# Performance work log

Measured on AMD Instinct MI355X. Metric: run time of the kernel, lower is better.

## Reference

```python
import jax, jax.numpy as jnp
import numpy as np

# Module constants (from init_kwargs)
K_BUDGET = 16      # selector budget K
R_REFRAC = 1       # refractory separation r
LAM = 0.5          # selector regularization lambda
MAX_PROXY = 64     # max_proxy_points (K_eff cap)


def setup_inputs() -> dict:
    key = jax.random.key(0)
    ks = jax.random.split(key, 8)
    B, T, D = 32, 4096, 128
    H, K_LIFT, D_MODEL = 256, 64, 1024
    g = lambda i, shape, s=0.05: jax.random.normal(ks[i], shape, jnp.float32) * s
    return {
        "x": jax.random.normal(ks[0], (B, T, D), jnp.float32),
        "W1": g(1, (D, H)),
        "b1": jnp.zeros((H,), jnp.float32),
        "w_e": g(2, (H,)),
        "w_s": g(3, (H,)),
        "W_lift": g(4, (D + 3, K_LIFT)),
        "b_lift": jnp.zeros((K_LIFT,), jnp.float32),
        "W_proj": g(5, (K_LIFT, D_MODEL)),
        "b_proj": jnp.zeros((D_MODEL,), jnp.float32),
        "log_temperature": jnp.zeros((), jnp.float32),
    }


def _soft_selector(saliency, log_temperature):
    """SoftSelectorProxy.forward: sigmoid relaxation of budget+refractory QP."""
    T = saliency.shape[1]
    temp = jnp.clip(jnp.exp(log_temperature), 0.1, 10.0)
    logits = (saliency / (2.0 * LAM) - 0.5) / temp
    y = jax.nn.sigmoid(logits)
    y = y.at[:, 0].set(0.0)
    budget = jnp.clip(y.sum(axis=1, keepdims=True), 1e-6)
    y = y * jnp.minimum(K_BUDGET / budget, 1.0)
    for d in range(1, min(R_REFRAC + 1, T)):  # r=1 -> single unrolled step
        pair_sum = y + jnp.roll(y, -d, axis=1)
        y = y * jnp.minimum(2.0 / (1.0 + pair_sum), 1.0)
    y = y.at[:, 0].set(0.0)
    return y


def reference(x, W1, b1, w_e, w_s, W_lift, b_lift, W_proj, b_proj, log_temperature):
    B, T, D = x.shape
    # 1. CausalEventModel: per-step MLP -> event scores + saliency  [B,T]
    h = jnp.tanh(jnp.einsum("btd,dh->bth", x, W1) + b1)
    event_scores = h @ w_e                       # [B,T] (unused downstream)
    saliency = jax.nn.softplus(h @ w_s)          # [B,T], nonnegative saliency
    # 2. Relaxed selector proxy -> continuous anchor weights y*  [B,T]
    y_star = _soft_selector(saliency, log_temperature)
    # 3. Dense anchor vectors: x augmented with 3 topology features (anchor_dim = D+3)
    tpos = jnp.broadcast_to(jnp.arange(T, dtype=x.dtype) / T, (B, T))
    cums = jnp.cumsum(saliency, axis=1)
    dense = jnp.concatenate(
        [x, saliency[..., None], tpos[..., None], cums[..., None]], axis=-1
    )  # [B,T,D+3]
    # 4. NormalizedLift: linear lift to k dims, L2-normalized cloud  [B,T,k]
    lifted = jnp.einsum("bta,ak->btk", dense, W_lift) + b_lift
    lifted = lifted / jnp.clip(
        jnp.linalg.norm(lifted, axis=-1, keepdims=True), 1e-6
    )
    # 5. Top-K anchor selection + gather + projection  [B,K_eff,d_model]
    K_eff = min(T, MAX_PROXY)
    _, top_idx = jax.lax.top_k(y_star, K_eff)                 # [B,K_eff]
    cloud = jnp.take_along_axis(lifted, top_idx[..., None], axis=1)  # [B,K_eff,k]
    tokens = jnp.einsum("bnk,kd->bnd", cloud, W_proj) + b_proj
    return tokens, y_star
```

## Files before the change

kernel.cpp:

```cpp
#include <hip/hip_runtime.h>
#include <math.h>

#define TT 4096
#define BB 32
#define DD 128
#define HH 256
#define KL 64
#define DM 1024
#define KEFF 64
#define KBUDGET 16.0f
#define LAM_ 0.5f

__global__ __launch_bounds__(256, 2) void k_sal(const float* __restrict__ x,
    const float* __restrict__ W1, const float* __restrict__ b1,
    const float* __restrict__ w_s, float* __restrict__ sal_out)
{
  __shared__ float xs[64][DD + 4];
  __shared__ float w1s[DD][64];

  const int tid = threadIdx.x;
  const long rowbase = (long)blockIdx.x * 64;

  {
    const float4* xg = (const float4*)(x + rowbase * DD);
    #pragma unroll
    for (int it = 0; it < 8; ++it) {
      int i = tid + it * 256;
      int r = i >> 5, c4 = i & 31;
      float4 v = xg[i];
      *(float4*)&xs[r][c4 * 4] = v;
    }
  }

  const int lane = tid & 63;
  const int wave = tid >> 6;
  const int hq = lane & 15;
  const int rq = lane >> 4;
  const int rb = wave * 16 + rq * 4;

  float s_acc[4] = {0.f, 0.f, 0.f, 0.f};

  for (int c = 0; c < HH / 64; ++c) {
    __syncthreads();
    #pragma unroll
    for (int it = 0; it < 8; ++it) {
      int i = tid + it * 256;
      int h4 = i & 15, d = i >> 4;
      float4 v = *(const float4*)&W1[d * HH + c * 64 + h4 * 4];
      *(float4*)&w1s[d][h4 * 4] = v;
    }
    __syncthreads();

    float acc[4][4];
    #pragma unroll
    for (int i = 0; i < 4; ++i)
      #pragma unroll
      for (int j = 0; j < 4; ++j) acc[i][j] = 0.f;

    #pragma unroll 2
    for (int d4 = 0; d4 < DD / 4; ++d4) {
      float4 xv0 = *(const float4*)&xs[rb + 0][d4 * 4];
      float4 xv1 = *(const float4*)&xs[rb + 1][d4 * 4];
      float4 xv2 = *(const float4*)&xs[rb + 2][d4 * 4];
      float4 xv3 = *(const float4*)&xs[rb + 3][d4 * 4];
      float4 wv0 = *(const float4*)&w1s[d4 * 4 + 0][hq * 4];
      float4 wv1 = *(const float4*)&w1s[d4 * 4 + 1][hq * 4];
      float4 wv2 = *(const float4*)&w1s[d4 * 4 + 2][hq * 4];
      float4 wv3 = *(const float4*)&w1s[d4 * 4 + 3][hq * 4];
#define ROWFMA(I, XV)                                  \
      acc[I][0] = fmaf(XV.x, wv0.x, acc[I][0]);        \
      acc[I][1] = fmaf(XV.x, wv0.y, acc[I][1]);        \
      acc[I][2] = fmaf(XV.x, wv0.z, acc[I][2]);        \
      acc[I][3] = fmaf(XV.x, wv0.w, acc[I][3]);        \
      acc[I][0] = fmaf(XV.y, wv1.x, acc[I][0]);        \
      acc[I][1] = fmaf(XV.y, wv1.y, acc[I][1]);        \
      acc[I][2] = fmaf(XV.y, wv1.z, acc[I][2]);        \
      acc[I][3] = fmaf(XV.y, wv1.w, acc[I][3]);        \
      acc[I][0] = fmaf(XV.z, wv2.x, acc[I][0]);        \
      acc[I][1] = fmaf(XV.z, wv2.y, acc[I][1]);        \
      acc[I][2] = fmaf(XV.z, wv2.z, acc[I][2]);        \
      acc[I][3] = fmaf(XV.z, wv2.w, acc[I][3]);        \
      acc[I][0] = fmaf(XV.w, wv3.x, acc[I][0]);        \
      acc[I][1] = fmaf(XV.w, wv3.y, acc[I][1]);        \
      acc[I][2] = fmaf(XV.w, wv3.z, acc[I][2]);        \
      acc[I][3] = fmaf(XV.w, wv3.w, acc[I][3]);
      ROWFMA(0, xv0)
      ROWFMA(1, xv1)
      ROWFMA(2, xv2)
      ROWFMA(3, xv3)
#undef ROWFMA
    }

    const int h0 = c * 64 + hq * 4;
    #pragma unroll
    for (int j = 0; j < 4; ++j) {
      float bj = b1[h0 + j];
      float wsj = w_s[h0 + j];
      #pragma unroll
      for (int i = 0; i < 4; ++i) {
        float t = tanhf(acc[i][j] + bj);
        s_acc[i] = fmaf(t, wsj, s_acc[i]);
      }
    }
  }

  #pragma unroll
  for (int m = 1; m < 16; m <<= 1) {
    #pragma unroll
    for (int i = 0; i < 4; ++i) s_acc[i] += __shfl_xor(s_acc[i], m, 64);
  }
  if (hq == 0) {
    #pragma unroll
    for (int i = 0; i < 4; ++i) {
      float z = s_acc[i];
      float sp = fmaxf(z, 0.f) + log1pf(expf(-fabsf(z)));
      sal_out[rowbase + rb + i] = sp;
    }
  }
}

__global__ __launch_bounds__(256) void k_sel(const float* __restrict__ logt,
    float* __restrict__ ysr, int* __restrict__ topidx,
    float* __restrict__ topsal, float* __restrict__ topcums)
{
  __shared__ float sal[TT];
  __shared__ float ya[TT];
  __shared__ float yb[TT];
  __shared__ float redf[8];
  __shared__ int   redi[8];

  const int tid = threadIdx.x;
  const int lane = tid & 63;
  const int wave = tid >> 6;
  const int b = blockIdx.x;
  float* row = ysr + (long)b * TT;

  for (int i = tid; i < TT; i += 256) sal[i] = row[i];
  __syncthreads();

  float temp = expf(logt[0]);
  temp = fminf(fmaxf(temp, 0.1f), 10.f);
  const float inv2lam = 1.0f / (2.0f * LAM_);

  for (int i = tid; i < TT; i += 256) {
    float z = (sal[i] * inv2lam - 0.5f) / temp;
    float s;
    if (z >= 0.f) { float e = expf(-z); s = 1.f / (1.f + e); }
    else          { float e = expf(z);  s = e / (1.f + e); }
    ya[i] = (i == 0) ? 0.f : s;
  }
  __syncthreads();

  float loc = 0.f;
  for (int i = tid; i < TT; i += 256) loc += ya[i];
  #pragma unroll
  for (int m = 1; m < 64; m <<= 1) loc += __shfl_xor(loc, m, 64);
  if (lane == 0) redf[wave] = loc;
  __syncthreads();
  float budget = redf[0] + redf[1] + redf[2] + redf[3];
  float scale = fminf(KBUDGET / fmaxf(budget, 1e-6f), 1.f);

  for (int i = tid; i < TT; i += 256) {
    float yi = ya[i] * scale;
    float yj = ya[(i + 1) & (TT - 1)] * scale;
    float m = fminf(2.f / (1.f + (yi + yj)), 1.f);
    yb[i] = (i == 0) ? 0.f : yi * m;
  }
  __syncthreads();

  for (int i = tid; i < TT; i += 256) row[i] = yb[i];

  const int base = tid * 16;
  float run = 0.f;
  #pragma unroll
  for (int j = 0; j < 16; ++j) { run += sal[base + j]; ya[base + j] = run; }
  float v = run;
  #pragma unroll
  for (int m = 1; m < 64; m <<= 1) {
    float u = __shfl_up(v, (unsigned)m, 64);
    if (lane >= m) v += u;
  }
  float lexcl = v - run;
  if (lane == 63) redf[4 + wave] = v;
  __syncthreads();
  float woff = 0.f;
  for (int w = 0; w < wave; ++w) woff += redf[4 + w];
  float off = woff + lexcl;
  #pragma unroll
  for (int j = 0; j < 16; ++j) ya[base + j] += off;
  __syncthreads();

  float lv[16];
  #pragma unroll
  for (int j = 0; j < 16; ++j) lv[j] = yb[base + j];
  unsigned rm = 0;
  float bv = -1.f; int bi = 1 << 30;
  #pragma unroll
  for (int j = 0; j < 16; ++j)
    if (!((rm >> j) & 1u) && lv[j] > bv) { bv = lv[j]; bi = base + j; }

  for (int it = 0; it < KEFF; ++it) {
    float cv = bv; int ci = bi;
    #pragma unroll
    for (int m = 1; m < 64; m <<= 1) {
      float ov = __shfl_xor(cv, m, 64);
      int   oi = __shfl_xor(ci, m, 64);
      if (ov > cv || (ov == cv && oi < ci)) { cv = ov; ci = oi; }
    }
    if (lane == 0) { redf[wave] = cv; redi[wave] = ci; }
    __syncthreads();
    float wv_ = redf[0]; int wi_ = redi[0];
    #pragma unroll
    for (int w = 1; w < 4; ++w)
      if (redf[w] > wv_ || (redf[w] == wv_ && redi[w] < wi_)) { wv_ = redf[w]; wi_ = redi[w]; }
    if (tid == 0) {
      topidx[b * KEFF + it]  = wi_;
      topsal[b * KEFF + it]  = sal[wi_];
      topcums[b * KEFF + it] = ya[wi_];
    }
    if (wi_ >= base && wi_ < base + 16) {
      rm |= 1u << (wi_ - base);
      bv = -1.f; bi = 1 << 30;
      #pragma unroll
      for (int j = 0; j < 16; ++j)
        if (!((rm >> j) & 1u) && lv[j] > bv) { bv = lv[j]; bi = base + j; }
    }
    __syncthreads();
  }
}

__global__ __launch_bounds__(256) void k_tok(const float* __restrict__ x,
    const float* __restrict__ W_lift, const float* __restrict__ b_lift,
    const float* __restrict__ W_proj, const float* __restrict__ b_proj,
    const int* __restrict__ topidx, const float* __restrict__ topsal,
    const float* __restrict__ topcums, float* __restrict__ tokens)
{
  __shared__ float cloud[8][KL];
  const int tid = threadIdx.x;
  const int k = tid & 63;
  const int g = tid >> 6;
  const int b = blockIdx.x >> 3;
  const int nb = (blockIdx.x & 7) * 8;

  #pragma unroll
  for (int a = 0; a < 2; ++a) {
    int n = nb + g + a * 4;
    int t = topidx[b * KEFF + n];
    const float* xr = x + ((long)b * TT + t) * DD;
    float acc = 0.f;
    #pragma unroll 8
    for (int d4 = 0; d4 < DD / 4; ++d4) {
      float4 xv = *(const float4*)&xr[d4 * 4];
      acc = fmaf(xv.x, W_lift[(d4 * 4 + 0) * KL + k], acc);
      acc = fmaf(xv.y, W_lift[(d4 * 4 + 1) * KL + k], acc);
      acc = fmaf(xv.z, W_lift[(d4 * 4 + 2) * KL + k], acc);
      acc = fmaf(xv.w, W_lift[(d4 * 4 + 3) * KL + k], acc);
    }
    float s  = topsal[b * KEFF + n];
    float tp = (float)t / (float)TT;
    float cm = topcums[b * KEFF + n];
    acc = fmaf(s,  W_lift[128 * KL + k], acc);
    acc = fmaf(tp, W_lift[129 * KL + k], acc);
    acc = fmaf(cm, W_lift[130 * KL + k], acc);
    acc += b_lift[k];
    float ss = acc * acc;
    #pragma unroll
    for (int m = 1; m < 64; m <<= 1) ss += __shfl_xor(ss, m, 64);
    float denom = fmaxf(sqrtf(ss), 1e-6f);
    cloud[g + a * 4][k] = acc / denom;
  }
  __syncthreads();

  #pragma unroll
  for (int q = 0; q < 4; ++q) {
    int dcol = tid + q * 256;
    float accp[8];
    #pragma unroll
    for (int n = 0; n < 8; ++n) accp[n] = 0.f;
    for (int kk = 0; kk < KL; ++kk) {
      float w = W_proj[kk * DM + dcol];
      #pragma unroll
      for (int n = 0; n < 8; ++n) accp[n] = fmaf(cloud[n][kk], w, accp[n]);
    }
    float bp = b_proj[dcol];
    #pragma unroll
    for (int n = 0; n < 8; ++n)
      tokens[((long)b * KEFF + nb + n) * DM + dcol] = accp[n] + bp;
  }
}

extern "C" void kernel_launch(void* const* d_in, const int* in_sizes, int n_in,
                              void* d_out, int out_size, void* d_ws, size_t ws_size,
                              hipStream_t stream) {
  const float* x      = (const float*)d_in[0];
  const float* W1     = (const float*)d_in[1];
  const float* b1     = (const float*)d_in[2];
  const float* w_s    = (const float*)d_in[4];
  const float* W_lift = (const float*)d_in[5];
  const float* b_lift = (const float*)d_in[6];
  const float* W_proj = (const float*)d_in[7];
  const float* b_proj = (const float*)d_in[8];
  const float* logt   = (const float*)d_in[9];

  float* tokens = (float*)d_out;
  float* ysr    = tokens + (size_t)BB * KEFF * DM;
  int*   topidx  = (int*)d_ws;
  float* topsal  = (float*)((char*)d_ws + 8192);
  float* topcums = (float*)((char*)d_ws + 16384);

  k_sal<<<(BB * TT) / 64, 256, 0, stream>>>(x, W1, b1, w_s, ysr);
  k_sel<<<BB, 256, 0, stream>>>(logt, ysr, topidx, topsal, topcums);
  k_tok<<<BB * 8, 256, 0, stream>>>(x, W_lift, b_lift, W_proj, b_proj,
                                    topidx, topsal, topcums, tokens);
}
```

Before: 266.7 us.

## Retile saliency MLP, use fast tanh, single-wave top-k, larger token blocks

The saliency kernel is retiled so each thread computes a 4x8 output block over half-H chunks with D staged in two halves. This shrinks shared memory enough to raise occupancy to 3 blocks per CU, and the per-thread partial sums are combined across waves through shared memory. tanhf is replaced with an exp2/rcp approximation to cut transcendental cost, which may slightly change numerics. The top-k selection now runs in a single wavefront with no block barriers per iteration, and the token kernel handles 16 anchors per block to reuse W_proj loads.

```diff
diff --git a/kernel.cpp b/kernel.cpp
--- a/kernel.cpp
+++ b/kernel.cpp
@@ -11,111 +11,122 @@
 #define KBUDGET 16.0f
 #define LAM_ 0.5f
 
-__global__ __launch_bounds__(256, 2) void k_sal(const float* __restrict__ x,
+__device__ __forceinline__ float fast_tanh(float x) {
+#if __has_builtin(__builtin_amdgcn_exp2f)
+  float e = __builtin_amdgcn_exp2f(x * 2.885390081777927f);
+#else
+  float e = __expf(2.0f * x);
+#endif
+  float r = __builtin_amdgcn_rcpf(e + 1.0f);
+  return fmaf(-2.0f, r, 1.0f);
+}
+
+__global__ __launch_bounds__(256, 3) void k_sal(const float* __restrict__ x,
     const float* __restrict__ W1, const float* __restrict__ b1,
     const float* __restrict__ w_s, float* __restrict__ sal_out)
 {
-  __shared__ float xs[64][DD + 4];
-  __shared__ float w1s[DD][64];
-
-  const int tid = threadIdx.x;
-  const long rowbase = (long)blockIdx.x * 64;
-
-  {
-    const float4* xg = (const float4*)(x + rowbase * DD);
-    #pragma unroll
-    for (int it = 0; it < 8; ++it) {
-      int i = tid + it * 256;
-      int r = i >> 5, c4 = i & 31;
-      float4 v = xg[i];
-      *(float4*)&xs[r][c4 * 4] = v;
-    }
-  }
-
+  __shared__ float xs[64][68];
+  __shared__ float w1s[64][128];
+  __shared__ float redsm[2][64];
+
+  const int tid  = threadIdx.x;
   const int lane = tid & 63;
   const int wave = tid >> 6;
-  const int hq = lane & 15;
-  const int rq = lane >> 4;
-  const int rb = wave * 16 + rq * 4;
+  const int wr = wave & 1;
+  const int wh = wave >> 1;
+  const int rq = lane >> 3;
+  const int hq = lane & 7;
+  const long rowbase = (long)blockIdx.x * 64;
 
   float s_acc[4] = {0.f, 0.f, 0.f, 0.f};
 
-  for (int c = 0; c < HH / 64; ++c) {
-    __syncthreads();
-    #pragma unroll
-    for (int it = 0; it < 8; ++it) {
-      int i = tid + it * 256;
-      int h4 = i & 15, d = i >> 4;
-      float4 v = *(const float4*)&W1[d * HH + c * 64 + h4 * 4];
-      *(float4*)&w1s[d][h4 * 4] = v;
-    }
-    __syncthreads();
-
-    float acc[4][4];
+  for (int hc = 0; hc < 2; ++hc) {
+    float acc[4][8];
     #pragma unroll
     for (int i = 0; i < 4; ++i)
       #pragma unroll
-      for (int j = 0; j < 4; ++j) acc[i][j] = 0.f;
-
-    #pragma unroll 2
-    for (int d4 = 0; d4 < DD / 4; ++d4) {
-      float4 xv0 = *(const float4*)&xs[rb + 0][d4 * 4];
-      float4 xv1 = *(const float4*)&xs[rb + 1][d4 * 4];
-      float4 xv2 = *(const float4*)&xs[rb + 2][d4 * 4];
-      float4 xv3 = *(const float4*)&xs[rb + 3][d4 * 4];
-      float4 wv0 = *(const float4*)&w1s[d4 * 4 + 0][hq * 4];
-      float4 wv1 = *(const float4*)&w1s[d4 * 4 + 1][hq * 4];
-      float4 wv2 = *(const float4*)&w1s[d4 * 4 + 2][hq * 4];
-      float4 wv3 = *(const float4*)&w1s[d4 * 4 + 3][hq * 4];
-#define ROWFMA(I, XV)                                  \
-      acc[I][0] = fmaf(XV.x, wv0.x, acc[I][0]);        \
-      acc[I][1] = fmaf(XV.x, wv0.y, acc[I][1]);        \
-      acc[I][2] = fmaf(XV.x, wv0.z, acc[I][2]);        \
-      acc[I][3] = fmaf(XV.x, wv0.w, acc[I][3]);        \
-      acc[I][0] = fmaf(XV.y, wv1.x, acc[I][0]);        \
-      acc[I][1] = fmaf(XV.y, wv1.y, acc[I][1]);        \
-      acc[I][2] = fmaf(XV.y, wv1.z, acc[I][2]);        \
-      acc[I][3] = fmaf(XV.y, wv1.w, acc[I][3]);        \
-      acc[I][0] = fmaf(XV.z, wv2.x, acc[I][0]);        \
-      acc[I][1] = fmaf(XV.z, wv2.y, acc[I][1]);        \
-      acc[I][2] = fmaf(XV.z, wv2.z, acc[I][2]);        \
-      acc[I][3] = fmaf(XV.z, wv2.w, acc[I][3]);        \
-      acc[I][0] = fmaf(XV.w, wv3.x, acc[I][0]);        \
-      acc[I][1] = fmaf(XV.w, wv3.y, acc[I][1]);        \
-      acc[I][2] = fmaf(XV.w, wv3.z, acc[I][2]);        \
-      acc[I][3] = fmaf(XV.w, wv3.w, acc[I][3]);
-      ROWFMA(0, xv0)
-      ROWFMA(1, xv1)
-      ROWFMA(2, xv2)
-      ROWFMA(3, xv3)
-#undef ROWFMA
-    }
-
-    const int h0 = c * 64 + hq * 4;
-    #pragma unroll
-    for (int j = 0; j < 4; ++j) {
-      float bj = b1[h0 + j];
+      for (int j = 0; j < 8; ++j) acc[i][j] = 0.f;
+
+    for (int ds = 0; ds < 2; ++ds) {
+      __syncthreads();
+      #pragma unroll
+      for (int p = 0; p < 4; ++p) {
+        int i = tid + p * 256;
+        int r = i >> 4, c4 = i & 15;
+        float4 v = *(const float4*)&x[(rowbase + r) * DD + ds * 64 + c4 * 4];
+        *(float4*)&xs[r][c4 * 4] = v;
+      }
+      #pragma unroll
+      for (int p = 0; p < 8; ++p) {
+        int i = tid + p * 256;
+        int h4 = i & 31, d = i >> 5;
+        float4 v = *(const float4*)&W1[(ds * 64 + d) * HH + hc * 128 + h4 * 4];
+        *(float4*)&w1s[d][h4 * 4] = v;
+      }
+      __syncthreads();
+
+      const int rbase = wr * 32 + rq;
+      const int hbase = wh * 64 + hq * 8;
+
+      #pragma unroll 4
+      for (int d4 = 0; d4 < 16; ++d4) {
+        float4 xv0 = *(const float4*)&xs[rbase +  0][d4 * 4];
+        float4 xv1 = *(const float4*)&xs[rbase +  8][d4 * 4];
+        float4 xv2 = *(const float4*)&xs[rbase + 16][d4 * 4];
+        float4 xv3 = *(const float4*)&xs[rbase + 24][d4 * 4];
+        #pragma unroll
+        for (int d = 0; d < 4; ++d) {
+          float4 wa = *(const float4*)&w1s[d4 * 4 + d][hbase];
+          float4 wb = *(const float4*)&w1s[d4 * 4 + d][hbase + 4];
+          float xd0 = (d == 0) ? xv0.x : (d == 1) ? xv0.y : (d == 2) ? xv0.z : xv0.w;
+          float xd1 = (d == 0) ? xv1.x : (d == 1) ? xv1.y : (d == 2) ? xv1.z : xv1.w;
+          float xd2 = (d == 0) ? xv2.x : (d == 1) ? xv2.y : (d == 2) ? xv2.z : xv2.w;
+          float xd3 = (d == 0) ? xv3.x : (d == 1) ? xv3.y : (d == 2) ? xv3.z : xv3.w;
+#define COLFMA(I, XD)                              \
+          acc[I][0] = fmaf(XD, wa.x, acc[I][0]);   \
+          acc[I][1] = fmaf(XD, wa.y, acc[I][1]);   \
+          acc[I][2] = fmaf(XD, wa.z, acc[I][2]);   \
+          acc[I][3] = fmaf(XD, wa.w, acc[I][3]);   \
+          acc[I][4] = fmaf(XD, wb.x, acc[I][4]);   \
+          acc[I][5] = fmaf(XD, wb.y, acc[I][5]);   \
+          acc[I][6] = fmaf(XD, wb.z, acc[I][6]);   \
+          acc[I][7] = fmaf(XD, wb.w, acc[I][7]);
+          COLFMA(0, xd0)
+          COLFMA(1, xd1)
+          COLFMA(2, xd2)
+          COLFMA(3, xd3)
+#undef COLFMA
+        }
+      }
+    }
+
+    const int h0 = hc * 128 + wh * 64 + hq * 8;
+    #pragma unroll
+    for (int j = 0; j < 8; ++j) {
+      float bj  = b1[h0 + j];
       float wsj = w_s[h0 + j];
       #pragma unroll
       for (int i = 0; i < 4; ++i) {
-        float t = tanhf(acc[i][j] + bj);
+        float t = fast_tanh(acc[i][j] + bj);
         s_acc[i] = fmaf(t, wsj, s_acc[i]);
       }
     }
   }
 
   #pragma unroll
-  for (int m = 1; m < 16; m <<= 1) {
+  for (int m = 1; m < 8; m <<= 1) {
     #pragma unroll
     for (int i = 0; i < 4; ++i) s_acc[i] += __shfl_xor(s_acc[i], m, 64);
   }
   if (hq == 0) {
     #pragma unroll
-    for (int i = 0; i < 4; ++i) {
-      float z = s_acc[i];
-      float sp = fmaxf(z, 0.f) + log1pf(expf(-fabsf(z)));
-      sal_out[rowbase + rb + i] = sp;
-    }
+    for (int i = 0; i < 4; ++i) redsm[wh][wr * 32 + rq + 8 * i] = s_acc[i];
+  }
+  __syncthreads();
+  if (tid < 64) {
+    float z = redsm[0][tid] + redsm[1][tid];
+    float sp = fmaxf(z, 0.f) + log1pf(expf(-fabsf(z)));
+    sal_out[rowbase + tid] = sp;
   }
 }
 
@@ -127,7 +138,6 @@
   __shared__ float ya[TT];
   __shared__ float yb[TT];
   __shared__ float redf[8];
-  __shared__ int   redi[8];
 
   const int tid = threadIdx.x;
   const int lane = tid & 63;
@@ -190,42 +200,35 @@
   for (int j = 0; j < 16; ++j) ya[base + j] += off;
   __syncthreads();
 
-  float lv[16];
-  #pragma unroll
-  for (int j = 0; j < 16; ++j) lv[j] = yb[base + j];
-  unsigned rm = 0;
-  float bv = -1.f; int bi = 1 << 30;
-  #pragma unroll
-  for (int j = 0; j < 16; ++j)
-    if (!((rm >> j) & 1u) && lv[j] > bv) { bv = lv[j]; bi = base + j; }
-
-  for (int it = 0; it < KEFF; ++it) {
-    float cv = bv; int ci = bi;
-    #pragma unroll
-    for (int m = 1; m < 64; m <<= 1) {
-      float ov = __shfl_xor(cv, m, 64);
-      int   oi = __shfl_xor(ci, m, 64);
-      if (ov > cv || (ov == cv && oi < ci)) { cv = ov; ci = oi; }
-    }
-    if (lane == 0) { redf[wave] = cv; redi[wave] = ci; }
-    __syncthreads();
-    float wv_ = redf[0]; int wi_ = redi[0];
-    #pragma unroll
-    for (int w = 1; w < 4; ++w)
-      if (redf[w] > wv_ || (redf[w] == wv_ && redi[w] < wi_)) { wv_ = redf[w]; wi_ = redi[w]; }
-    if (tid == 0) {
-      topidx[b * KEFF + it]  = wi_;
-      topsal[b * KEFF + it]  = sal[wi_];
-      topcums[b * KEFF + it] = ya[wi_];
-    }
-    if (wi_ >= base && wi_ < base + 16) {
-      rm |= 1u << (wi_ - base);
-      bv = -1.f; bi = 1 << 30;
-      #pragma unroll
-      for (int j = 0; j < 16; ++j)
-        if (!((rm >> j) & 1u) && lv[j] > bv) { bv = lv[j]; bi = base + j; }
-    }
-    __syncthreads();
+  if (wave == 0) {
+    const int b2 = lane * 64;
+    float bv = -1.f; int bi = 1 << 30;
+    for (int j = 0; j < 64; ++j) {
+      float vv = yb[b2 + j];
+      if (vv > bv) { bv = vv; bi = b2 + j; }
+    }
+    for (int it = 0; it < KEFF; ++it) {
+      float cv = bv; int ci = bi;
+      #pragma unroll
+      for (int m = 1; m < 64; m <<= 1) {
+        float ov = __shfl_xor(cv, m, 64);
+        int   oi = __shfl_xor(ci, m, 64);
+        if (ov > cv || (ov == cv && oi < ci)) { cv = ov; ci = oi; }
+      }
+      if (lane == 0) {
+        topidx[b * KEFF + it]  = ci;
+        topsal[b * KEFF + it]  = sal[ci];
+        topcums[b * KEFF + it] = ya[ci];
+      }
+      if (ci >= b2 && ci < b2 + 64) {
+        yb[ci] = -1.f;
+        bv = -1.f; bi = 1 << 30;
+        for (int j = 0; j < 64; ++j) {
+          float vv = yb[b2 + j];
+          if (vv > bv) { bv = vv; bi = b2 + j; }
+        }
+      }
+    }
   }
 }
 
@@ -235,15 +238,15 @@
     const int* __restrict__ topidx, const float* __restrict__ topsal,
     const float* __restrict__ topcums, float* __restrict__ tokens)
 {
-  __shared__ float cloud[8][KL];
+  __shared__ float cloud[16][KL];
   const int tid = threadIdx.x;
   const int k = tid & 63;
   const int g = tid >> 6;
-  const int b = blockIdx.x >> 3;
-  const int nb = (blockIdx.x & 7) * 8;
-
-  #pragma unroll
-  for (int a = 0; a < 2; ++a) {
+  const int b = blockIdx.x >> 2;
+  const int nb = (blockIdx.x & 3) * 16;
+
+  #pragma unroll
+  for (int a = 0; a < 4; ++a) {
     int n = nb + g + a * 4;
     int t = topidx[b * KEFF + n];
     const float* xr = x + ((long)b * TT + t) * DD;
@@ -274,17 +277,18 @@
   #pragma unroll
   for (int q = 0; q < 4; ++q) {
     int dcol = tid + q * 256;
-    float accp[8];
-    #pragma unroll
-    for (int n = 0; n < 8; ++n) accp[n] = 0.f;
+    float accp[16];
+    #pragma unroll
+    for (int n = 0; n < 16; ++n) accp[n] = 0.f;
+    #pragma unroll 4
     for (int kk = 0; kk < KL; ++kk) {
       float w = W_proj[kk * DM + dcol];
       #pragma unroll
-      for (int n = 0; n < 8; ++n) accp[n] = fmaf(cloud[n][kk], w, accp[n]);
+      for (int n = 0; n < 16; ++n) accp[n] = fmaf(cloud[n][kk], w, accp[n]);
     }
     float bp = b_proj[dcol];
     #pragma unroll
-    for (int n = 0; n < 8; ++n)
+    for (int n = 0; n < 16; ++n)
       tokens[((long)b * KEFF + nb + n) * DM + dcol] = accp[n] + bp;
   }
 }
@@ -310,6 +314,6 @@
 
   k_sal<<<(BB * TT) / 64, 256, 0, stream>>>(x, W1, b1, w_s, ysr);
   k_sel<<<BB, 256, 0, stream>>>(logt, ysr, topidx, topsal, topcums);
-  k_tok<<<BB * 8, 256, 0, stream>>>(x, W_lift, b_lift, W_proj, b_proj,
+  k_tok<<<BB * 4, 256, 0, stream>>>(x, W_lift, b_lift, W_proj, b_proj,
                                     topidx, topsal, topcums, tokens);
 }
```

Result: faster. 261.0 us (-2.1%).
